# Kernel optimization log

Measured on AMD Instinct MI355X. Metric: run time of the kernel, lower is better.

Reference implementation:

```python
import jax, jax.numpy as jnp
import numpy as np

N_HEAD = 16
D_MODEL = 1024
D_K = 64
D_V = 64
LN_EPS = 1e-6


def setup_inputs() -> dict:
    key = jax.random.key(0)
    ks = jax.random.split(key, 10)
    B, S = 2, 2048
    scale = 0.02
    return {
        "q": jax.random.normal(ks[0], (B, S, D_MODEL), jnp.float32),
        "k": jax.random.normal(ks[1], (B, S, D_MODEL), jnp.float32),
        "v": jax.random.normal(ks[2], (B, S, D_MODEL), jnp.float32),
        "Wq": jax.random.normal(ks[3], (D_MODEL, N_HEAD * D_K), jnp.float32) * scale,
        "Wk": jax.random.normal(ks[4], (D_MODEL, N_HEAD * D_K), jnp.float32) * scale,
        "Wv": jax.random.normal(ks[5], (D_MODEL, N_HEAD * D_V), jnp.float32) * scale,
        "Wfc": jax.random.normal(ks[6], (N_HEAD * D_V, D_MODEL), jnp.float32) * scale,
        "bfc": jnp.zeros((D_MODEL,), jnp.float32),
        "gamma": jnp.ones((D_MODEL,), jnp.float32),
        "beta": jnp.zeros((D_MODEL,), jnp.float32),
    }


def reference(q, k, v, Wq, Wk, Wv, Wfc, bfc, gamma, beta):
    B, S, _ = q.shape
    residual = q
    # QKV projections, split into heads: [B, S, H, Dh]
    qh = (q @ Wq).reshape(B, S, N_HEAD, D_K)
    kh = (k @ Wk).reshape(B, S, N_HEAD, D_K)
    vh = (v @ Wv).reshape(B, S, N_HEAD, D_V)
    # scaled dot-product attention (explicit score matrix, as in source)
    temperature = jnp.asarray(D_K, qh.dtype) ** 0.5
    attn = jnp.einsum("bqhd,bkhd->bhqk", qh, kh) / temperature
    attn = jax.nn.softmax(attn, axis=-1)
    out = jnp.einsum("bhqk,bkhd->bqhd", attn, vh).reshape(B, S, N_HEAD * D_V)
    # output projection (dropout is identity in eval mode)
    out = out @ Wfc + bfc
    # residual + layernorm (eps=1e-6)
    x = out + residual
    mu = jnp.mean(x, axis=-1, keepdims=True)
    var = jnp.mean(jnp.square(x - mu), axis=-1, keepdims=True)
    return (x - mu) / jnp.sqrt(var + LN_EPS) * gamma + beta
```

## Files before the change

kernel.cpp:

```cpp
#include <hip/hip_runtime.h>

typedef float f32x4 __attribute__((ext_vector_type(4)));
typedef short short8 __attribute__((ext_vector_type(8)));
typedef short short4v __attribute__((ext_vector_type(4)));
typedef unsigned short ushort_t;

#define D_MODEL 1024
#define N_HEAD 16
#define SEQ 2048
#define BATCH 2
#define M_TOK 4096
#define HD 1024
#define NT 32
#define QSCALE_L2E 0.1803368801111f

__device__ __forceinline__ ushort_t f2bf(float f) {
    union { float f; unsigned int u; } x; x.f = f;
    unsigned int r = x.u + 0x7fffu + ((x.u >> 16) & 1u);
    return (ushort_t)(r >> 16);
}
__device__ __forceinline__ ushort_t f2bf_fast(float f) {
    union { float f; unsigned int u; } x; x.f = f;
    return (ushort_t)((x.u + 0x8000u) >> 16);
}

__device__ __forceinline__ void async_copy16(const ushort_t* gptr, ushort_t* lptr) {
    __builtin_amdgcn_global_load_lds(
        (const __attribute__((address_space(1))) unsigned int*)gptr,
        (__attribute__((address_space(3))) unsigned int*)lptr, 16, 0, 0);
}

__global__ __launch_bounds__(256) void prep_fused(const float* __restrict__ w0,
                                                  const float* __restrict__ w1,
                                                  const float* __restrict__ w2,
                                                  const float* __restrict__ w3,
                                                  ushort_t* __restrict__ o0,
                                                  ushort_t* __restrict__ o1,
                                                  ushort_t* __restrict__ o2,
                                                  ushort_t* __restrict__ o3,
                                                  const float* __restrict__ q,
                                                  const float* __restrict__ k,
                                                  const float* __restrict__ v,
                                                  ushort_t* __restrict__ qo,
                                                  ushort_t* __restrict__ ko,
                                                  ushort_t* __restrict__ vo) {
    const int z = blockIdx.z;
    const int tid = threadIdx.x;
    const int flat = blockIdx.x + 64 * blockIdx.y;
    if (z < 4) {
        if (flat >= 1024) return;
        const int R = D_MODEL, C = D_MODEL;
        const float* in = (z == 0) ? w0 : (z == 1) ? w1 : (z == 2) ? w2 : w3;
        ushort_t* out = (z == 0) ? o0 : (z == 1) ? o1 : (z == 2) ? o2 : o3;
        __shared__ ushort_t t[32][33];
        int bc = (flat & 31) * 32, br = (flat >> 5) * 32;
        int tx = tid & 31, ty = tid >> 5;
        for (int i = ty; i < 32; i += 8)
            t[i][tx] = f2bf(in[(size_t)(br + i) * C + bc + tx]);
        __syncthreads();
        for (int i = ty; i < 32; i += 8)
            out[(size_t)(bc + i) * R + br + tx] = t[tx][i];
    } else {
        const float* s = (z == 4) ? q : (z == 5) ? k : v;
        ushort_t* d = (z == 4) ? qo : (z == 5) ? ko : vo;
        size_t i = ((size_t)flat * 256 + tid) * 8;
        float4 a = *(const float4*)(s + i);
        float4 b = *(const float4*)(s + i + 4);
        ushort_t tmp[8] = {f2bf(a.x), f2bf(a.y), f2bf(a.z), f2bf(a.w),
                           f2bf(b.x), f2bf(b.y), f2bf(b.z), f2bf(b.w)};
        *(short8*)(d + i) = *(short8*)tmp;
    }
}

__global__ __launch_bounds__(256) void gemm_qkv(const ushort_t* __restrict__ qb,
                                                const ushort_t* __restrict__ kb,
                                                const ushort_t* __restrict__ vb,
                                                const ushort_t* __restrict__ wq,
                                                const ushort_t* __restrict__ wk,
                                                const ushort_t* __restrict__ wv,
                                                ushort_t* __restrict__ Qo,
                                                ushort_t* __restrict__ Ko,
                                                ushort_t* __restrict__ VtO) {
    __shared__ ushort_t As[128 * 32];
    __shared__ ushort_t Bs[128 * 32];
    const int z = blockIdx.z;
    const ushort_t* A = (z == 0) ? qb : (z == 1) ? kb : vb;
    const ushort_t* Bt = (z == 0) ? wq : (z == 1) ? wk : wv;
    const int tid = threadIdx.x;
    const int wave = tid >> 6, lane = tid & 63;
    const int quad = lane >> 4, l16 = lane & 15;
    const int m0 = blockIdx.y * 128, n0 = blockIdx.x * 128;
    const int wm = (wave >> 1) * 64, wn = (wave & 1) * 64;
    const int K = D_MODEL, N = D_MODEL;

    f32x4 acc[4][4];
    for (int i = 0; i < 4; ++i)
        for (int j = 0; j < 4; ++j) acc[i][j] = (f32x4){0.f, 0.f, 0.f, 0.f};

    for (int kk = 0; kk < K; kk += 32) {
        __syncthreads();
        #pragma unroll
        for (int c = 0; c < 2; ++c) {
            int flat = ((wave * 2 + c) * 64 + lane) * 8;
            int r = flat >> 5, col = flat & 31;
            async_copy16(Bt + (size_t)(n0 + r) * K + kk + col, &Bs[(wave * 2 + c) * 512]);
            async_copy16(A + (size_t)(m0 + r) * K + kk + col, &As[(wave * 2 + c) * 512]);
        }
        __syncthreads();
        short8 af[4], bfr[4];
        #pragma unroll
        for (int i = 0; i < 4; ++i)
            af[i] = *(const short8*)&As[(wm + i * 16 + l16) * 32 + quad * 8];
        #pragma unroll
        for (int j = 0; j < 4; ++j)
            bfr[j] = *(const short8*)&Bs[(wn + j * 16 + l16) * 32 + quad * 8];
        #pragma unroll
        for (int i = 0; i < 4; ++i)
            #pragma unroll
            for (int j = 0; j < 4; ++j)
                acc[i][j] = __builtin_amdgcn_mfma_f32_16x16x32_bf16(af[i], bfr[j], acc[i][j], 0, 0, 0);
    }
    if (z == 2) {
        #pragma unroll
        for (int i = 0; i < 4; ++i)
            #pragma unroll
            for (int j = 0; j < 4; ++j) {
                int n = n0 + wn + j * 16 + l16;
                int mBase = m0 + wm + i * 16;
                int quadR = (quad + (n >> 2)) & 3;
                ushort_t tmp[4];
                #pragma unroll
                for (int r = 0; r < 4; ++r) tmp[r] = f2bf(acc[i][j][r]);
                *(short4v*)&VtO[(size_t)n * M_TOK + mBase + quadR * 4] = *(short4v*)tmp;
            }
    } else {
        ushort_t* C = (z == 0) ? Qo : Ko;
        const float scale = (z == 0) ? QSCALE_L2E : 1.0f;
        #pragma unroll
        for (int i = 0; i < 4; ++i)
            #pragma unroll
            for (int j = 0; j < 4; ++j) {
                int n = n0 + wn + j * 16 + l16;
                #pragma unroll
                for (int r = 0; r < 4; ++r) {
                    int m = m0 + wm + i * 16 + quad * 4 + r;
                    C[(size_t)m * N + n] = f2bf(acc[i][j][r] * scale);
                }
            }
    }
}

__global__ __launch_bounds__(256) void gemm_fc(const ushort_t* __restrict__ A,
                                               const ushort_t* __restrict__ Bt,
                                               float* __restrict__ Cf,
                                               const float* __restrict__ bias,
                                               const float* __restrict__ resid) {
    __shared__ ushort_t As[128 * 32];
    __shared__ ushort_t Bs[64 * 32];
    const int tid = threadIdx.x;
    const int wave = tid >> 6, lane = tid & 63;
    const int quad = lane >> 4, l16 = lane & 15;
    const int m0 = blockIdx.y * 128, n0 = blockIdx.x * 64;
    const int K = D_MODEL, N = D_MODEL;

    f32x4 acc[2][4];
    for (int i = 0; i < 2; ++i)
        for (int j = 0; j < 4; ++j) acc[i][j] = (f32x4){0.f, 0.f, 0.f, 0.f};

    for (int kk = 0; kk < K; kk += 32) {
        __syncthreads();
        #pragma unroll
        for (int c = 0; c < 2; ++c) {
            int g = wave * 2 + c;
            int flat = (g * 64 + lane) * 8;
            int r = flat >> 5, col = flat & 31;
            async_copy16(A + (size_t)(m0 + r) * K + kk + col, &As[g * 512]);
        }
        {
            int flat = (wave * 64 + lane) * 8;
            int r = flat >> 5, col = flat & 31;
            async_copy16(Bt + (size_t)(n0 + r) * K + kk + col, &Bs[wave * 512]);
        }
        __syncthreads();
        short8 af[2], bfr[4];
        #pragma unroll
        for (int i = 0; i < 2; ++i)
            af[i] = *(const short8*)&As[(wave * 32 + i * 16 + l16) * 32 + quad * 8];
        #pragma unroll
        for (int j = 0; j < 4; ++j)
            bfr[j] = *(const short8*)&Bs[(j * 16 + l16) * 32 + quad * 8];
        #pragma unroll
        for (int i = 0; i < 2; ++i)
            #pragma unroll
            for (int j = 0; j < 4; ++j)
                acc[i][j] = __builtin_amdgcn_mfma_f32_16x16x32_bf16(af[i], bfr[j], acc[i][j], 0, 0, 0);
    }
    #pragma unroll
    for (int i = 0; i < 2; ++i)
        #pragma unroll
        for (int j = 0; j < 4; ++j) {
            int n = n0 + j * 16 + l16;
            #pragma unroll
            for (int r = 0; r < 4; ++r) {
                int m = m0 + wave * 32 + i * 16 + quad * 4 + r;
                Cf[(size_t)m * N + n] = acc[i][j][r] + bias[n] + resid[(size_t)m * N + n];
            }
        }
}

__global__ __launch_bounds__(256, 3) void attn64(const ushort_t* __restrict__ Qh,
                                                 const ushort_t* __restrict__ Kh,
                                                 const ushort_t* __restrict__ Vt,
                                                 ushort_t* __restrict__ O) {
    __shared__ __align__(16) char smem[25600];
    const int tid = threadIdx.x;
    const int wave = tid >> 6, lane = tid & 63;
    const int quad = lane >> 4, l16 = lane & 15;
    const int h = blockIdx.x, b = blockIdx.y, qt = blockIdx.z;
    const size_t base = (size_t)b * SEQ * HD + h * 64;
    const ushort_t* Qb = Qh + base + (size_t)(qt * 64) * HD;
    const ushort_t* Kb = Kh + base;
    const ushort_t* Vb = Vt + (size_t)(h * 64) * M_TOK + (size_t)b * SEQ;

    ushort_t* Vw = (ushort_t*)smem + wave * 3072;
    float* lsb = (float*)(smem + 24576);

    short8 qf[4][2];
    #pragma unroll
    for (int nt = 0; nt < 4; ++nt)
        #pragma unroll
        for (int s = 0; s < 2; ++s)
            qf[nt][s] = *(const short8*)(Qb + (size_t)(nt * 16 + l16) * HD + s * 32 + quad * 8);

    f32x4 oacc[4][4];
    #pragma unroll
    for (int nt = 0; nt < 4; ++nt)
        #pragma unroll
        for (int dt = 0; dt < 4; ++dt) oacc[nt][dt] = (f32x4){0.f, 0.f, 0.f, 0.f};
    float lsum[4] = {0.f, 0.f, 0.f, 0.f};

    const ushort_t* Kr = Kb + (size_t)(wave * 16 + l16) * HD + quad * 8;
    const ushort_t* Vg = Vb + (size_t)(lane >> 1) * M_TOK + wave * 16 + (lane & 1) * 8;
    ushort_t* VLd = Vw + lane * 8;

    short8 kf0[2], kf1[2];
    #pragma unroll
    for (int s = 0; s < 2; ++s) kf0[s] = *(const short8*)(Kr + s * 32);
    #pragma unroll
    for (int c = 0; c < 2; ++c)
        async_copy16(Vg + (size_t)c * 32 * M_TOK, VLd + c * 512);
    #pragma unroll
    for (int c = 0; c < 2; ++c)
        async_copy16(Vg + (size_t)c * 32 * M_TOK + 64, VLd + 1024 + c * 512);

    ushort_t *vb0 = Vw, *vb1 = Vw + 1024, *vb2 = Vw + 2048;
    const int rot = (l16 >> 2) & 3;

    for (int kt = 0; kt < NT; ++kt) {
        if (kt == NT - 1) __builtin_amdgcn_s_waitcnt(0x0F70);
        else              __builtin_amdgcn_s_waitcnt(0x0F72);

        if (kt + 1 < NT) {
            #pragma unroll
            for (int s = 0; s < 2; ++s)
                kf1[s] = *(const short8*)(Kr + (size_t)(kt + 1) * 64 * HD + s * 32);
        }
        if (kt + 2 < NT) {
            #pragma unroll
            for (int c = 0; c < 2; ++c)
                async_copy16(Vg + (size_t)c * 32 * M_TOK + (kt + 2) * 64, vb2 + lane * 8 + c * 512);
        }

        short4v vf[4];
        #pragma unroll
        for (int dt = 0; dt < 4; ++dt)
            vf[dt] = *(const short4v*)&vb0[(dt * 16 + l16) * 16 + (((quad + rot) & 3) * 4)];

        f32x4 sacc[4];
        #pragma unroll
        for (int nt = 0; nt < 4; ++nt) sacc[nt] = (f32x4){0.f, 0.f, 0.f, 0.f};
        #pragma unroll
        for (int s = 0; s < 2; ++s)
            #pragma unroll
            for (int nt = 0; nt < 4; ++nt)
                sacc[nt] = __builtin_amdgcn_mfma_f32_16x16x32_bf16(kf0[s], qf[nt][s], sacc[nt], 0, 0, 0);

        short4v pf[4];
        #pragma unroll
        for (int nt = 0; nt < 4; ++nt) {
            ushort_t tmp[4];
            #pragma unroll
            for (int i = 0; i < 4; ++i) {
                float pv = __builtin_amdgcn_exp2f(sacc[nt][i]);
                lsum[nt] += pv;
                tmp[i] = f2bf_fast(pv);
            }
            pf[nt] = *(short4v*)tmp;
        }
        #pragma unroll
        for (int nt = 0; nt < 4; ++nt)
            #pragma unroll
            for (int dt = 0; dt < 4; ++dt)
                oacc[nt][dt] = __builtin_amdgcn_mfma_f32_16x16x16bf16_1k(pf[nt], vf[dt], oacc[nt][dt], 0, 0, 0);

        kf0[0] = kf1[0]; kf0[1] = kf1[1];
        ushort_t* t = vb0; vb0 = vb1; vb1 = vb2; vb2 = t;
    }

    #pragma unroll
    for (int nt = 0; nt < 4; ++nt) {
        lsum[nt] += __shfl_xor(lsum[nt], 16, 64);
        lsum[nt] += __shfl_xor(lsum[nt], 32, 64);
    }
    if (quad == 0) {
        #pragma unroll
        for (int nt = 0; nt < 4; ++nt) lsb[wave * 64 + nt * 16 + l16] = lsum[nt];
    }
    __syncthreads();

    float* R = (float*)smem;
    #pragma unroll
    for (int w = 0; w < 4; ++w) {
        if (wave == w) {
            #pragma unroll
            for (int nt = 0; nt < 4; ++nt)
                #pragma unroll
                for (int dt = 0; dt < 4; ++dt)
                    #pragma unroll
                    for (int i = 0; i < 4; ++i) {
                        int idx = (nt * 16 + quad * 4 + i) * 66 + dt * 16 + l16;
                        if (w == 0) R[idx] = oacc[nt][dt][i];
                        else        R[idx] += oacc[nt][dt][i];
                    }
        }
        __syncthreads();
    }
    float inv[4];
    #pragma unroll
    for (int i = 0; i < 4; ++i) {
        int qrow = wave * 16 + quad * 4 + i;
        float t = lsb[qrow] + lsb[64 + qrow] + lsb[128 + qrow] + lsb[192 + qrow];
        inv[i] = 1.f / t;
    }
    ushort_t* Ob = O + base + (size_t)(qt * 64) * HD;
    #pragma unroll
    for (int i = 0; i < 4; ++i) {
        int qrow = wave * 16 + quad * 4 + i;
        #pragma unroll
        for (int dt = 0; dt < 4; ++dt) {
            int d = dt * 16 + l16;
            Ob[(size_t)qrow * HD + d] = f2bf(R[qrow * 66 + d] * inv[i]);
        }
    }
}

__global__ __launch_bounds__(256) void ln_kernel(float* __restrict__ x,
                                                 const float* __restrict__ gamma,
                                                 const float* __restrict__ beta) {
    const int D = D_MODEL;
    float* xr = x + (size_t)blockIdx.x * D;
    const int tid = threadIdx.x;
    float4 v = *(const float4*)(xr + tid * 4);
    float s = v.x + v.y + v.z + v.w;
    float s2 = v.x * v.x + v.y * v.y + v.z * v.z + v.w * v.w;
    #pragma unroll
    for (int off = 1; off < 64; off <<= 1) {
        s += __shfl_xor(s, off, 64);
        s2 += __shfl_xor(s2, off, 64);
    }
    __shared__ float ws1[4], ws2[4];
    int wave = tid >> 6, lane = tid & 63;
    if (lane == 0) { ws1[wave] = s; ws2[wave] = s2; }
    __syncthreads();
    s = ws1[0] + ws1[1] + ws1[2] + ws1[3];
    s2 = ws2[0] + ws2[1] + ws2[2] + ws2[3];
    float mean = s * (1.f / D);
    float var = s2 * (1.f / D) - mean * mean;
    float rstd = rsqrtf(var + 1e-6f);
    float4 g = *(const float4*)(gamma + tid * 4);
    float4 bt = *(const float4*)(beta + tid * 4);
    float4 o;
    o.x = (v.x - mean) * rstd * g.x + bt.x;
    o.y = (v.y - mean) * rstd * g.y + bt.y;
    o.z = (v.z - mean) * rstd * g.z + bt.z;
    o.w = (v.w - mean) * rstd * g.w + bt.w;
    *(float4*)(xr + tid * 4) = o;
}

extern "C" void kernel_launch(void* const* d_in, const int* in_sizes, int n_in,
                              void* d_out, int out_size, void* d_ws, size_t ws_size,
                              hipStream_t stream) {
    const float* q = (const float*)d_in[0];
    const float* k = (const float*)d_in[1];
    const float* v = (const float*)d_in[2];
    const float* Wq = (const float*)d_in[3];
    const float* Wk = (const float*)d_in[4];
    const float* Wv = (const float*)d_in[5];
    const float* Wfc = (const float*)d_in[6];
    const float* bfc = (const float*)d_in[7];
    const float* gamma = (const float*)d_in[8];
    const float* beta = (const float*)d_in[9];
    float* out = (float*)d_out;

    char* ws = (char*)d_ws;
    const size_t MB = 1u << 20;
    ushort_t* WqT  = (ushort_t*)(ws + 0 * MB);
    ushort_t* WkT  = (ushort_t*)(ws + 2 * MB);
    ushort_t* WvT  = (ushort_t*)(ws + 4 * MB);
    ushort_t* WfcT = (ushort_t*)(ws + 6 * MB);
    ushort_t* qb   = (ushort_t*)(ws + 8 * MB);
    ushort_t* kb   = (ushort_t*)(ws + 16 * MB);
    ushort_t* vb   = (ushort_t*)(ws + 24 * MB);
    ushort_t* Qh   = (ushort_t*)(ws + 32 * MB);
    ushort_t* Kh   = (ushort_t*)(ws + 40 * MB);
    ushort_t* Vt   = (ushort_t*)(ws + 48 * MB);
    ushort_t* Oh   = (ushort_t*)(ws + 8 * MB);

    const int M = M_TOK, D = D_MODEL;
    prep_fused<<<dim3(64, 32, 7), 256, 0, stream>>>(
        Wq, Wk, Wv, Wfc, WqT, WkT, WvT, WfcT, q, k, v, qb, kb, vb);

    gemm_qkv<<<dim3(D / 128, M / 128, 3), 256, 0, stream>>>(qb, kb, vb, WqT, WkT, WvT, Qh, Kh, Vt);

    attn64<<<dim3(N_HEAD, BATCH, SEQ / 64), 256, 0, stream>>>(Qh, Kh, Vt, Oh);

    gemm_fc<<<dim3(D / 64, M / 128), 256, 0, stream>>>(Oh, WfcT, out, bfc, q);

    ln_kernel<<<M, 256, 0, stream>>>(out, gamma, beta);
}
```

Before: 254.1 us.

## Store GEMM operands and V in K-paneled tiled layouts for contiguous loads

Converts activations, weights, and the attention output into K-panel layouts of 32 columns each, so every 128x32 GEMM tile is one contiguous block in memory. The QKV and FC GEMMs now load two K-panels per barrier pair (K step 64), which halves the number of synchronisations. V is written in a per-head, per-batch, per-key-tile blocked layout so the attention kernel's async V loads are contiguous. The layout changes touch producers and consumers across several kernels and double the GEMM shared memory use.

```diff
diff --git a/kernel.cpp b/kernel.cpp
--- a/kernel.cpp
+++ b/kernel.cpp
@@ -12,6 +12,8 @@
 #define M_TOK 4096
 #define HD 1024
 #define NT 32
+#define APANEL 131072
+#define WPANEL 32768
 #define QSCALE_L2E 0.1803368801111f
 
 __device__ __forceinline__ ushort_t f2bf(float f) {
@@ -49,7 +51,7 @@
     const int flat = blockIdx.x + 64 * blockIdx.y;
     if (z < 4) {
         if (flat >= 1024) return;
-        const int R = D_MODEL, C = D_MODEL;
+        const int C = D_MODEL;
         const float* in = (z == 0) ? w0 : (z == 1) ? w1 : (z == 2) ? w2 : w3;
         ushort_t* out = (z == 0) ? o0 : (z == 1) ? o1 : (z == 2) ? o2 : o3;
         __shared__ ushort_t t[32][33];
@@ -58,17 +60,19 @@
         for (int i = ty; i < 32; i += 8)
             t[i][tx] = f2bf(in[(size_t)(br + i) * C + bc + tx]);
         __syncthreads();
+        size_t pbase = (size_t)(br >> 5) * WPANEL;
         for (int i = ty; i < 32; i += 8)
-            out[(size_t)(bc + i) * R + br + tx] = t[tx][i];
+            out[pbase + (size_t)(bc + i) * 32 + tx] = t[tx][i];
     } else {
         const float* s = (z == 4) ? q : (z == 5) ? k : v;
         ushort_t* d = (z == 4) ? qo : (z == 5) ? ko : vo;
         size_t i = ((size_t)flat * 256 + tid) * 8;
+        int m = (int)(i >> 10), k0 = (int)(i & 1023);
         float4 a = *(const float4*)(s + i);
         float4 b = *(const float4*)(s + i + 4);
         ushort_t tmp[8] = {f2bf(a.x), f2bf(a.y), f2bf(a.z), f2bf(a.w),
                            f2bf(b.x), f2bf(b.y), f2bf(b.z), f2bf(b.w)};
-        *(short8*)(d + i) = *(short8*)tmp;
+        *(short8*)(d + (size_t)(k0 >> 5) * APANEL + (size_t)m * 32 + (k0 & 31)) = *(short8*)tmp;
     }
 }
 
@@ -80,9 +84,9 @@
                                                 const ushort_t* __restrict__ wv,
                                                 ushort_t* __restrict__ Qo,
                                                 ushort_t* __restrict__ Ko,
-                                                ushort_t* __restrict__ VtO) {
-    __shared__ ushort_t As[128 * 32];
-    __shared__ ushort_t Bs[128 * 32];
+                                                ushort_t* __restrict__ V4) {
+    __shared__ ushort_t As[2][128 * 32];
+    __shared__ ushort_t Bs[2][128 * 32];
     const int z = blockIdx.z;
     const ushort_t* A = (z == 0) ? qb : (z == 1) ? kb : vb;
     const ushort_t* Bt = (z == 0) ? wq : (z == 1) ? wk : wv;
@@ -91,47 +95,61 @@
     const int quad = lane >> 4, l16 = lane & 15;
     const int m0 = blockIdx.y * 128, n0 = blockIdx.x * 128;
     const int wm = (wave >> 1) * 64, wn = (wave & 1) * 64;
-    const int K = D_MODEL, N = D_MODEL;
+    const int N = D_MODEL;
 
     f32x4 acc[4][4];
     for (int i = 0; i < 4; ++i)
         for (int j = 0; j < 4; ++j) acc[i][j] = (f32x4){0.f, 0.f, 0.f, 0.f};
 
-    for (int kk = 0; kk < K; kk += 32) {
-        __syncthreads();
-        #pragma unroll
-        for (int c = 0; c < 2; ++c) {
-            int flat = ((wave * 2 + c) * 64 + lane) * 8;
-            int r = flat >> 5, col = flat & 31;
-            async_copy16(Bt + (size_t)(n0 + r) * K + kk + col, &Bs[(wave * 2 + c) * 512]);
-            async_copy16(A + (size_t)(m0 + r) * K + kk + col, &As[(wave * 2 + c) * 512]);
-        }
-        __syncthreads();
-        short8 af[4], bfr[4];
+    for (int it = 0; it < 16; ++it) {
+        __syncthreads();
+        const ushort_t* Ap = A + (size_t)(it * 2) * APANEL + (size_t)m0 * 32;
+        const ushort_t* Bp = Bt + (size_t)(it * 2) * WPANEL + (size_t)n0 * 32;
+        #pragma unroll
+        for (int hf = 0; hf < 2; ++hf) {
+            #pragma unroll
+            for (int c = 0; c < 2; ++c) {
+                int off = (wave * 2 + c) * 512;
+                async_copy16(Ap + hf * APANEL + off + lane * 8, &As[hf][off] + lane * 8);
+                async_copy16(Bp + hf * WPANEL + off + lane * 8, &Bs[hf][off] + lane * 8);
+            }
+        }
+        __syncthreads();
+        short8 af[4][2], bfr[4][2];
         #pragma unroll
         for (int i = 0; i < 4; ++i)
-            af[i] = *(const short8*)&As[(wm + i * 16 + l16) * 32 + quad * 8];
+            #pragma unroll
+            for (int sk = 0; sk < 2; ++sk)
+                af[i][sk] = *(const short8*)&As[sk][(wm + i * 16 + l16) * 32 + quad * 8];
         #pragma unroll
         for (int j = 0; j < 4; ++j)
-            bfr[j] = *(const short8*)&Bs[(wn + j * 16 + l16) * 32 + quad * 8];
-        #pragma unroll
-        for (int i = 0; i < 4; ++i)
-            #pragma unroll
-            for (int j = 0; j < 4; ++j)
-                acc[i][j] = __builtin_amdgcn_mfma_f32_16x16x32_bf16(af[i], bfr[j], acc[i][j], 0, 0, 0);
+            #pragma unroll
+            for (int sk = 0; sk < 2; ++sk)
+                bfr[j][sk] = *(const short8*)&Bs[sk][(wn + j * 16 + l16) * 32 + quad * 8];
+        #pragma unroll
+        for (int sk = 0; sk < 2; ++sk)
+            #pragma unroll
+            for (int i = 0; i < 4; ++i)
+                #pragma unroll
+                for (int j = 0; j < 4; ++j)
+                    acc[i][j] = __builtin_amdgcn_mfma_f32_16x16x32_bf16(af[i][sk], bfr[j][sk], acc[i][j], 0, 0, 0);
     }
     if (z == 2) {
+        const int tile64 = m0 + wm;
+        const int b2 = tile64 >> 11;
+        const int kt = (tile64 & 2047) >> 6;
         #pragma unroll
         for (int i = 0; i < 4; ++i)
             #pragma unroll
             for (int j = 0; j < 4; ++j) {
                 int n = n0 + wn + j * 16 + l16;
-                int mBase = m0 + wm + i * 16;
-                int quadR = (quad + (n >> 2)) & 3;
+                int h2 = n >> 6, d = n & 63;
+                int quadR = (quad + ((n >> 2) & 3)) & 3;
                 ushort_t tmp[4];
                 #pragma unroll
                 for (int r = 0; r < 4; ++r) tmp[r] = f2bf(acc[i][j][r]);
-                *(short4v*)&VtO[(size_t)n * M_TOK + mBase + quadR * 4] = *(short4v*)tmp;
+                size_t dst = ((((size_t)(h2 * 2 + b2) * NT + kt) * 4 + i) << 10) + d * 16 + quadR * 4;
+                *(short4v*)&V4[dst] = *(short4v*)tmp;
             }
     } else {
         ushort_t* C = (z == 0) ? Qo : Ko;
@@ -155,45 +173,53 @@
                                                float* __restrict__ Cf,
                                                const float* __restrict__ bias,
                                                const float* __restrict__ resid) {
-    __shared__ ushort_t As[128 * 32];
-    __shared__ ushort_t Bs[64 * 32];
+    __shared__ ushort_t As[2][128 * 32];
+    __shared__ ushort_t Bs[2][64 * 32];
     const int tid = threadIdx.x;
     const int wave = tid >> 6, lane = tid & 63;
     const int quad = lane >> 4, l16 = lane & 15;
     const int m0 = blockIdx.y * 128, n0 = blockIdx.x * 64;
-    const int K = D_MODEL, N = D_MODEL;
+    const int N = D_MODEL;
 
     f32x4 acc[2][4];
     for (int i = 0; i < 2; ++i)
         for (int j = 0; j < 4; ++j) acc[i][j] = (f32x4){0.f, 0.f, 0.f, 0.f};
 
-    for (int kk = 0; kk < K; kk += 32) {
-        __syncthreads();
+    for (int it = 0; it < 16; ++it) {
+        __syncthreads();
+        const ushort_t* Ap = A + (size_t)(it * 2) * APANEL + (size_t)m0 * 32;
+        const ushort_t* Bp = Bt + (size_t)(it * 2) * WPANEL + (size_t)n0 * 32;
+        #pragma unroll
+        for (int c = 0; c < 4; ++c) {
+            int g = wave * 4 + c;
+            int sk = g >> 3, off = (g & 7) * 512;
+            async_copy16(Ap + sk * APANEL + off + lane * 8, &As[sk][off] + lane * 8);
+        }
         #pragma unroll
         for (int c = 0; c < 2; ++c) {
             int g = wave * 2 + c;
-            int flat = (g * 64 + lane) * 8;
-            int r = flat >> 5, col = flat & 31;
-            async_copy16(A + (size_t)(m0 + r) * K + kk + col, &As[g * 512]);
-        }
-        {
-            int flat = (wave * 64 + lane) * 8;
-            int r = flat >> 5, col = flat & 31;
-            async_copy16(Bt + (size_t)(n0 + r) * K + kk + col, &Bs[wave * 512]);
-        }
-        __syncthreads();
-        short8 af[2], bfr[4];
+            int sk = g >> 2, off = (g & 3) * 512;
+            async_copy16(Bp + sk * WPANEL + off + lane * 8, &Bs[sk][off] + lane * 8);
+        }
+        __syncthreads();
+        short8 af[2][2], bfr[4][2];
         #pragma unroll
         for (int i = 0; i < 2; ++i)
-            af[i] = *(const short8*)&As[(wave * 32 + i * 16 + l16) * 32 + quad * 8];
+            #pragma unroll
+            for (int sk = 0; sk < 2; ++sk)
+                af[i][sk] = *(const short8*)&As[sk][(wave * 32 + i * 16 + l16) * 32 + quad * 8];
         #pragma unroll
         for (int j = 0; j < 4; ++j)
-            bfr[j] = *(const short8*)&Bs[(j * 16 + l16) * 32 + quad * 8];
-        #pragma unroll
-        for (int i = 0; i < 2; ++i)
-            #pragma unroll
-            for (int j = 0; j < 4; ++j)
-                acc[i][j] = __builtin_amdgcn_mfma_f32_16x16x32_bf16(af[i], bfr[j], acc[i][j], 0, 0, 0);
+            #pragma unroll
+            for (int sk = 0; sk < 2; ++sk)
+                bfr[j][sk] = *(const short8*)&Bs[sk][(j * 16 + l16) * 32 + quad * 8];
+        #pragma unroll
+        for (int sk = 0; sk < 2; ++sk)
+            #pragma unroll
+            for (int i = 0; i < 2; ++i)
+                #pragma unroll
+                for (int j = 0; j < 4; ++j)
+                    acc[i][j] = __builtin_amdgcn_mfma_f32_16x16x32_bf16(af[i][sk], bfr[j][sk], acc[i][j], 0, 0, 0);
     }
     #pragma unroll
     for (int i = 0; i < 2; ++i)
@@ -210,7 +236,7 @@
 
 __global__ __launch_bounds__(256, 3) void attn64(const ushort_t* __restrict__ Qh,
                                                  const ushort_t* __restrict__ Kh,
-                                                 const ushort_t* __restrict__ Vt,
+                                                 const ushort_t* __restrict__ V4,
                                                  ushort_t* __restrict__ O) {
     __shared__ __align__(16) char smem[25600];
     const int tid = threadIdx.x;
@@ -220,7 +246,7 @@
     const size_t base = (size_t)b * SEQ * HD + h * 64;
     const ushort_t* Qb = Qh + base + (size_t)(qt * 64) * HD;
     const ushort_t* Kb = Kh + base;
-    const ushort_t* Vb = Vt + (size_t)(h * 64) * M_TOK + (size_t)b * SEQ;
+    const ushort_t* Vg = V4 + (((size_t)(h * 2 + b) * NT * 4) + wave) * 1024 + lane * 8;
 
     ushort_t* Vw = (ushort_t*)smem + wave * 3072;
     float* lsb = (float*)(smem + 24576);
@@ -240,18 +266,15 @@
     float lsum[4] = {0.f, 0.f, 0.f, 0.f};
 
     const ushort_t* Kr = Kb + (size_t)(wave * 16 + l16) * HD + quad * 8;
-    const ushort_t* Vg = Vb + (size_t)(lane >> 1) * M_TOK + wave * 16 + (lane & 1) * 8;
     ushort_t* VLd = Vw + lane * 8;
 
     short8 kf0[2], kf1[2];
     #pragma unroll
     for (int s = 0; s < 2; ++s) kf0[s] = *(const short8*)(Kr + s * 32);
     #pragma unroll
-    for (int c = 0; c < 2; ++c)
-        async_copy16(Vg + (size_t)c * 32 * M_TOK, VLd + c * 512);
-    #pragma unroll
-    for (int c = 0; c < 2; ++c)
-        async_copy16(Vg + (size_t)c * 32 * M_TOK + 64, VLd + 1024 + c * 512);
+    for (int c = 0; c < 2; ++c) async_copy16(Vg + c * 512, VLd + c * 512);
+    #pragma unroll
+    for (int c = 0; c < 2; ++c) async_copy16(Vg + 4096 + c * 512, VLd + 1024 + c * 512);
 
     ushort_t *vb0 = Vw, *vb1 = Vw + 1024, *vb2 = Vw + 2048;
     const int rot = (l16 >> 2) & 3;
@@ -268,7 +291,7 @@
         if (kt + 2 < NT) {
             #pragma unroll
             for (int c = 0; c < 2; ++c)
-                async_copy16(Vg + (size_t)c * 32 * M_TOK + (kt + 2) * 64, vb2 + lane * 8 + c * 512);
+                async_copy16(Vg + (size_t)(kt + 2) * 4096 + c * 512, vb2 + lane * 8 + c * 512);
         }
 
         short4v vf[4];
@@ -342,14 +365,15 @@
         float t = lsb[qrow] + lsb[64 + qrow] + lsb[128 + qrow] + lsb[192 + qrow];
         inv[i] = 1.f / t;
     }
-    ushort_t* Ob = O + base + (size_t)(qt * 64) * HD;
     #pragma unroll
     for (int i = 0; i < 4; ++i) {
         int qrow = wave * 16 + quad * 4 + i;
+        size_t tok = (size_t)b * SEQ + qt * 64 + qrow;
         #pragma unroll
         for (int dt = 0; dt < 4; ++dt) {
             int d = dt * 16 + l16;
-            Ob[(size_t)qrow * HD + d] = f2bf(R[qrow * 66 + d] * inv[i]);
+            size_t dst = (size_t)(h * 2 + (dt >> 1)) * APANEL + tok * 32 + (dt & 1) * 16 + l16;
+            O[dst] = f2bf(R[qrow * 66 + d] * inv[i]);
         }
     }
 }
```

After: 241.7 us. 1.05x faster.
